# Kernel tuning notes

Hardware: AMD Instinct MI355X
Metric: run time of the kernel (lower is better)

## Reference

```python
import jax, jax.numpy as jnp
import numpy as np

E = 16          # num_experts
H = 2048        # hidden_size
I = 768         # moe_intermediate_size
T = 2048        # tokens (batch*seq)
K = 2           # top_k


def setup_inputs() -> dict:
    key = jax.random.key(0)
    k1, k2, k3, k4, k5 = jax.random.split(key, 5)
    hidden_states = jax.random.normal(k1, (T, H), dtype=jnp.float32)
    top_k_index = jax.random.randint(k2, (T, K), 0, E, dtype=jnp.int32)
    w = jax.random.uniform(k3, (T, K), dtype=jnp.float32)
    top_k_weights = w / jnp.sum(w, axis=-1, keepdims=True)  # softmax-like router weights
    init_std = 0.02
    gate_up_proj = jax.random.normal(k4, (E, 2 * I, H), dtype=jnp.float32) * init_std
    down_proj = jax.random.normal(k5, (E, H, I), dtype=jnp.float32) * init_std
    return {
        "hidden_states": hidden_states,
        "top_k_index": top_k_index,
        "top_k_weights": top_k_weights,
        "gate_up_proj": gate_up_proj,
        "down_proj": down_proj,
    }


def reference(hidden_states, top_k_index, top_k_weights, gate_up_proj, down_proj):
    # Combine matrix C[t, e] = sum_k top_k_weights[t, k] * 1[top_k_index[t,k] == e]
    # Tokens not routed to expert e get weight 0, so the dense-masked compute
    # below is mathematically identical to the per-expert gather/scatter loop.
    t_idx = jnp.arange(T)[:, None]
    C = jnp.zeros((T, E), dtype=hidden_states.dtype).at[t_idx, top_k_index].add(top_k_weights)

    # gate/up projection for every (token, expert): [T, E, 2I]
    gu = jnp.einsum('th,egh->teg', hidden_states, gate_up_proj)
    gate, up = jnp.split(gu, 2, axis=-1)                  # [T, E, I] each
    mid = jax.nn.silu(gate) * up                          # SwiGLU, [T, E, I]
    # down projection fused with routed combine weights -> [T, H]
    out = jnp.einsum('tei,ehi,te->th', mid, down_proj, C)
    return out
```

## Files before the change

### kernel.cpp

```cpp
#include <hip/hip_runtime.h>

#define TTOK  2048
#define HID   2048
#define IMID  768
#define NEXP  16
#define NPAIR 4096
#define NSLOT 4224
#define BM    128
#define BK    64
#define MAXT  48
#define ABUF  (128 * 64)

#define GUP_CHUNKS 24576
#define DN_CHUNKS  12288

typedef __attribute__((ext_vector_type(8))) short  short8;
typedef __attribute__((ext_vector_type(4))) float  floatx4;

__device__ __forceinline__ unsigned pk2(float a, float b) {
    union { float f; unsigned u; } x{a}, y{b};
    unsigned ra = (x.u + 0x7FFFu + ((x.u >> 16) & 1u)) >> 16;
    unsigned rb = (y.u + 0x7FFFu + ((y.u >> 16) & 1u)) & 0xFFFF0000u;
    return ra | rb;
}

__device__ __forceinline__ short f2bf(float f) {
    union { float f; unsigned u; } v; v.f = f;
    return (short)((v.u + 0x7FFFu + ((v.u >> 16) & 1u)) >> 16);
}

__device__ __forceinline__ short8 cvt8(float4 a, float4 b) {
    union { unsigned u[4]; short8 s; } r;
    r.u[0] = pk2(a.x, a.y); r.u[1] = pk2(a.z, a.w);
    r.u[2] = pk2(b.x, b.y); r.u[3] = pk2(b.z, b.w);
    return r.s;
}

__device__ __forceinline__ void async_cp16(const void* g, void* l) {
    __builtin_amdgcn_global_load_lds(
        (const __attribute__((address_space(1))) void*)g,
        (__attribute__((address_space(3))) void*)l, 16, 0, 0);
}

__global__ __launch_bounds__(256) void k_pre(
    const float* __restrict__ hs, const int* __restrict__ idx,
    const float* __restrict__ tkw, const float* __restrict__ gup,
    const float* __restrict__ down, int* __restrict__ ntiles,
    int4* __restrict__ tiles, int* __restrict__ tok,
    float* __restrict__ wgt, short* __restrict__ X,
    short* __restrict__ gupb, short* __restrict__ downb)
{
    const int tid = threadIdx.x;
    const int bx  = (int)blockIdx.x;
    if (bx == 0) {
        __shared__ int cnt[NEXP], cur[NEXP];
        if (tid < NEXP) cnt[tid] = 0;
        __syncthreads();
        for (int i = tid; i < NPAIR; i += 256) atomicAdd(&cnt[idx[i]], 1);
        __syncthreads();
        if (tid == 0) {
            int s = 0, nt = 0;
            for (int e = 0; e < NEXP; e++) {
                cur[e] = s;
                int n = cnt[e];
                for (int tt = 0; tt * BM < n; tt++) {
                    tiles[nt] = make_int4(e, s + tt * BM, min(BM, n - tt * BM), 0);
                    nt++;
                }
                s += n;
            }
            *ntiles = nt;
        }
        __syncthreads();
        for (int i = tid; i < NPAIR; i += 256) {
            int e = idx[i];
            int p = atomicAdd(&cur[e], 1);
            tok[p] = i >> 1;
            wgt[p] = tkw[i];
        }
        for (int i = NPAIR + tid; i < NSLOT; i += 256) { tok[i] = 0; wgt[i] = 0.0f; }
    } else if (bx <= TTOK) {
        const int row = bx - 1;
        const float* src = hs + (size_t)row * HID + tid * 8;
        float4 a = *(const float4*)src;
        float4 b = *(const float4*)(src + 4);
        *(short8*)(X + (size_t)row * HID + tid * 8) = cvt8(a, b);
    } else if (bx <= TTOK + GUP_CHUNKS) {
        const size_t c = (size_t)(bx - 1 - TTOK);
        const float* src = gup + c * 2048 + tid * 8;
        float4 a = *(const float4*)src;
        float4 b = *(const float4*)(src + 4);
        *(short8*)(gupb + c * 2048 + tid * 8) = cvt8(a, b);
    } else {
        const size_t c = (size_t)(bx - 1 - TTOK - GUP_CHUNKS);
        const float* src = down + c * 2048 + tid * 8;
        float4 a = *(const float4*)src;
        float4 b = *(const float4*)(src + 4);
        *(short8*)(downb + c * 2048 + tid * 8) = cvt8(a, b);
    }
}

__global__ __launch_bounds__(256, 2) void k_gemm1(
    const short* __restrict__ gupb, const short* __restrict__ X,
    const int* __restrict__ ntiles, const int4* __restrict__ tiles,
    const int* __restrict__ tok, const float* __restrict__ wgt,
    short* __restrict__ mid)
{
    if ((int)blockIdx.y >= *ntiles) return;
    const int4 td = tiles[blockIdx.y];
    const int e = td.x, rowstart = td.y, nvalid = td.z;
    const int ct = blockIdx.x;

    __shared__ short sA[2 * ABUF];
    __shared__ short sB[2 * ABUF];
    __shared__ int   s_tok[BM];
    __shared__ float s_w[BM];

    const int tid = threadIdx.x;
    if (tid < BM) { s_tok[tid] = tok[rowstart + tid]; s_w[tid] = wgt[rowstart + tid]; }
    __syncthreads();

    const int wave = tid >> 6, lane = tid & 63;
    const int m16 = lane & 15, quad = lane >> 4;

    const int lrow = tid >> 3;
    const int gsw  = (tid & 7) ^ (lrow & 7);
    const short* aga[4];
    const short* bga[4];
#pragma unroll
    for (int j = 0; j < 4; j++)
        aga[j] = X + (size_t)s_tok[lrow + j * 32] * HID + gsw * 8;
    const short* gb = gupb + (size_t)e * (2 * IMID) * HID + gsw * 8;
#pragma unroll
    for (int j = 0; j < 2; j++) {
        bga[j]     = gb + (size_t)(ct * 64 + lrow + j * 32) * HID;
        bga[j + 2] = gb + (size_t)(IMID + ct * 64 + lrow + j * 32) * HID;
    }

    auto stage = [&](int k0, short* dA, short* dB) {
#pragma unroll
        for (int j = 0; j < 4; j++)
            async_cp16(aga[j] + k0, dA + j * 2048 + wave * 512);
#pragma unroll
        for (int j = 0; j < 4; j++)
            async_cp16(bga[j] + k0, dB + j * 2048 + wave * 512);
    };

    const int Wm = (wave >> 1) << 6;
    const int Wi = (wave & 1) << 5;
    floatx4 ag[4][2], au[4][2];
#pragma unroll
    for (int a = 0; a < 4; a++)
#pragma unroll
        for (int b = 0; b < 2; b++) { ag[a][b] = (floatx4)0.0f; au[a][b] = (floatx4)0.0f; }

    stage(0, sA, sB);
    __syncthreads();

    const int nsteps = HID / BK;
    for (int ks = 0; ks < nsteps; ks++) {
        const short* Acur = sA + (ks & 1) * ABUF;
        const short* Bcur = sB + (ks & 1) * ABUF;
        if (ks + 1 < nsteps)
            stage((ks + 1) * BK, sA + ((ks + 1) & 1) * ABUF, sB + ((ks + 1) & 1) * ABUF);

#pragma unroll
        for (int h = 0; h < 2; h++) {
            short8 af[4];
#pragma unroll
            for (int mf = 0; mf < 4; mf++) {
                int row = Wm + mf * 16 + m16;
                int gc = (h * 4 + quad) ^ (row & 7);
                af[mf] = *(const short8*)&Acur[row * 64 + gc * 8];
            }
#pragma unroll
            for (int nf = 0; nf < 2; nf++) {
                int brow = Wi + nf * 16 + m16;
                int gcb = (h * 4 + quad) ^ (brow & 7);
                const short8 bg = *(const short8*)&Bcur[brow * 64 + gcb * 8];
                const short8 bu = *(const short8*)&Bcur[(64 + brow) * 64 + gcb * 8];
#pragma unroll
                for (int mf = 0; mf < 4; mf++) {
                    ag[mf][nf] = __builtin_amdgcn_mfma_f32_16x16x32_bf16(af[mf], bg, ag[mf][nf], 0, 0, 0);
                    au[mf][nf] = __builtin_amdgcn_mfma_f32_16x16x32_bf16(af[mf], bu, au[mf][nf], 0, 0, 0);
                }
            }
        }
        __syncthreads();
    }

#pragma unroll
    for (int mf = 0; mf < 4; mf++) {
#pragma unroll
        for (int r = 0; r < 4; r++) {
            int m = Wm + mf * 16 + quad * 4 + r;
            if (m < nvalid) {
                float w = s_w[m];
                size_t rowp = (size_t)(rowstart + m) * IMID + ct * 64;
#pragma unroll
                for (int nf = 0; nf < 2; nf++) {
                    float g = ag[mf][nf][r], u = au[mf][nf][r];
                    float val = g / (1.0f + __expf(-g)) * u * w;
                    mid[rowp + Wi + nf * 16 + m16] = f2bf(val);
                }
            }
        }
    }
}

__global__ __launch_bounds__(256, 2) void k_gemm2(
    const short* __restrict__ downb, const short* __restrict__ mid,
    const int* __restrict__ ntiles, const int4* __restrict__ tiles,
    const int* __restrict__ tok, float* __restrict__ out)
{
    if ((int)blockIdx.y >= *ntiles) return;
    const int4 td = tiles[blockIdx.y];
    const int e = td.x, rowstart = td.y, nvalid = td.z;
    const int ct = blockIdx.x;

    __shared__ short sA[2 * ABUF];
    __shared__ short sB[2 * ABUF];
    __shared__ int   s_tok[BM];

    const int tid = threadIdx.x;
    if (tid < BM) s_tok[tid] = tok[rowstart + tid];
    __syncthreads();

    const int wave = tid >> 6, lane = tid & 63;
    const int m16 = lane & 15, quad = lane >> 4;

    const int lrow = tid >> 3;
    const int gsw  = (tid & 7) ^ (lrow & 7);
    const short* aga[4];
    const short* bga[4];
#pragma unroll
    for (int j = 0; j < 4; j++)
        aga[j] = mid + (size_t)(rowstart + lrow + j * 32) * IMID + gsw * 8;
    const short* db = downb + ((size_t)e * HID + ct * 128) * IMID + gsw * 8;
#pragma unroll
    for (int j = 0; j < 4; j++)
        bga[j] = db + (size_t)(lrow + j * 32) * IMID;

    auto stage = [&](int k0, short* dA, short* dB) {
#pragma unroll
        for (int j = 0; j < 4; j++)
            async_cp16(aga[j] + k0, dA + j * 2048 + wave * 512);
#pragma unroll
        for (int j = 0; j < 4; j++)
            async_cp16(bga[j] + k0, dB + j * 2048 + wave * 512);
    };

    const int Wm = (wave >> 1) << 6;
    const int Wn = (wave & 1) << 6;
    floatx4 acc[4][4];
#pragma unroll
    for (int a = 0; a < 4; a++)
#pragma unroll
        for (int b = 0; b < 4; b++) acc[a][b] = (floatx4)0.0f;

    stage(0, sA, sB);
    __syncthreads();

    const int nsteps = IMID / BK;
    for (int ks = 0; ks < nsteps; ks++) {
        const short* Acur = sA + (ks & 1) * ABUF;
        const short* Bcur = sB + (ks & 1) * ABUF;
        if (ks + 1 < nsteps)
            stage((ks + 1) * BK, sA + ((ks + 1) & 1) * ABUF, sB + ((ks + 1) & 1) * ABUF);

#pragma unroll
        for (int h = 0; h < 2; h++) {
            short8 af[4];
#pragma unroll
            for (int mf = 0; mf < 4; mf++) {
                int row = Wm + mf * 16 + m16;
                int gc = (h * 4 + quad) ^ (row & 7);
                af[mf] = *(const short8*)&Acur[row * 64 + gc * 8];
            }
#pragma unroll
            for (int nf = 0; nf < 4; nf++) {
                int brow = Wn + nf * 16 + m16;
                int gcb = (h * 4 + quad) ^ (brow & 7);
                const short8 bf_ = *(const short8*)&Bcur[brow * 64 + gcb * 8];
#pragma unroll
                for (int mf = 0; mf < 4; mf++)
                    acc[mf][nf] = __builtin_amdgcn_mfma_f32_16x16x32_bf16(af[mf], bf_, acc[mf][nf], 0, 0, 0);
            }
        }
        __syncthreads();
    }

#pragma unroll
    for (int mf = 0; mf < 4; mf++) {
#pragma unroll
        for (int r = 0; r < 4; r++) {
            int m = Wm + mf * 16 + quad * 4 + r;
            if (m < nvalid) {
                int t = s_tok[m];
                float* op = out + (size_t)t * HID + ct * 128;
#pragma unroll
                for (int nf = 0; nf < 4; nf++)
                    atomicAdd(op + Wn + nf * 16 + m16, acc[mf][nf][r]);
            }
        }
    }
}

extern "C" void kernel_launch(void* const* d_in, const int* in_sizes, int n_in,
                              void* d_out, int out_size, void* d_ws, size_t ws_size,
                              hipStream_t stream) {
    const float* hs   = (const float*)d_in[0];
    const int*   idx  = (const int*)d_in[1];
    const float* tkw  = (const float*)d_in[2];
    const float* gup  = (const float*)d_in[3];
    const float* down = (const float*)d_in[4];
    float* out = (float*)d_out;

    char* ws = (char*)d_ws;
    int*   ntiles = (int*)ws;
    int4*  tiles  = (int4*)(ws + 16);
    int*   tok    = (int*)(ws + 1024);
    float* wgt    = (float*)(ws + 1024 + NSLOT * 4);
    short* mid    = (short*)(ws + 36864);
    short* X      = (short*)(ws + 36864 + (size_t)NSLOT * IMID * 2);
    short* gupb   = (short*)(ws + (16u << 20));
    short* downb  = (short*)(ws + (16u << 20) + (size_t)NEXP * 2 * IMID * HID * 2);

    hipMemsetAsync(d_out, 0, (size_t)TTOK * HID * sizeof(float), stream);
    k_pre  <<<1 + TTOK + GUP_CHUNKS + DN_CHUNKS, 256, 0, stream>>>(
        hs, idx, tkw, gup, down, ntiles, tiles, tok, wgt, X, gupb, downb);
    k_gemm1<<<dim3(IMID / 64, MAXT), 256, 0, stream>>>(gupb, X, ntiles, tiles, tok, wgt, mid);
    k_gemm2<<<dim3(HID / 128, MAXT), 256, 0, stream>>>(downb, mid, ntiles, tiles, tok, out);
}
```

Measured before the change: 484.0 us.

## Use grid-stride conversion kernel and explicit vmcnt waits with raw barriers in GEMMs

The fp32-to-bf16 preprocessing kernel changes from one block per 2048-element chunk (about 39k blocks) to a fixed 2048-block grid-stride loop over all three tensors. Both grouped GEMM loops replace __syncthreads with explicit s_waitcnt vmcnt(8)/vmcnt(0) plus s_barrier and sched_barrier. This lets the prefetch of the next K tile stay in flight while waiting only for the current tile's async LDS loads. The aim is to cut block-launch overhead and over-conservative waits, but correctness now depends on the hand-set vmcnt count matching the 8 async copies per stage.

```diff
diff --git a/kernel.cpp b/kernel.cpp
--- a/kernel.cpp
+++ b/kernel.cpp
@@ -11,8 +11,10 @@
 #define MAXT  48
 #define ABUF  (128 * 64)
 
-#define GUP_CHUNKS 24576
-#define DN_CHUNKS  12288
+#define HS_U   524288u
+#define GUP_U  6291456u
+#define DN_U   3145728u
+#define NU_TOT (HS_U + GUP_U + DN_U)
 
 typedef __attribute__((ext_vector_type(8))) short  short8;
 typedef __attribute__((ext_vector_type(4))) float  floatx4;
@@ -51,8 +53,7 @@
     short* __restrict__ gupb, short* __restrict__ downb)
 {
     const int tid = threadIdx.x;
-    const int bx  = (int)blockIdx.x;
-    if (bx == 0) {
+    if (blockIdx.x == 0) {
         __shared__ int cnt[NEXP], cur[NEXP];
         if (tid < NEXP) cnt[tid] = 0;
         __syncthreads();
@@ -79,24 +80,18 @@
             wgt[p] = tkw[i];
         }
         for (int i = NPAIR + tid; i < NSLOT; i += 256) { tok[i] = 0; wgt[i] = 0.0f; }
-    } else if (bx <= TTOK) {
-        const int row = bx - 1;
-        const float* src = hs + (size_t)row * HID + tid * 8;
-        float4 a = *(const float4*)src;
-        float4 b = *(const float4*)(src + 4);
-        *(short8*)(X + (size_t)row * HID + tid * 8) = cvt8(a, b);
-    } else if (bx <= TTOK + GUP_CHUNKS) {
-        const size_t c = (size_t)(bx - 1 - TTOK);
-        const float* src = gup + c * 2048 + tid * 8;
-        float4 a = *(const float4*)src;
-        float4 b = *(const float4*)(src + 4);
-        *(short8*)(gupb + c * 2048 + tid * 8) = cvt8(a, b);
-    } else {
-        const size_t c = (size_t)(bx - 1 - TTOK - GUP_CHUNKS);
-        const float* src = down + c * 2048 + tid * 8;
-        float4 a = *(const float4*)src;
-        float4 b = *(const float4*)(src + 4);
-        *(short8*)(downb + c * 2048 + tid * 8) = cvt8(a, b);
+        return;
+    }
+    const unsigned nthr = (gridDim.x - 1) * 256u;
+    unsigned u = (blockIdx.x - 1) * 256u + tid;
+    for (; u < NU_TOT; u += nthr) {
+        const float* src; short* dst; unsigned off;
+        if (u < HS_U)              { src = hs;   dst = X;     off = u; }
+        else if (u < HS_U + GUP_U) { src = gup;  dst = gupb;  off = u - HS_U; }
+        else                       { src = down; dst = downb; off = u - HS_U - GUP_U; }
+        float4 a = *((const float4*)src + (size_t)2 * off);
+        float4 b = *((const float4*)src + (size_t)2 * off + 1);
+        *((short8*)dst + off) = cvt8(a, b);
     }
 }
 
@@ -155,14 +150,19 @@
         for (int b = 0; b < 2; b++) { ag[a][b] = (floatx4)0.0f; au[a][b] = (floatx4)0.0f; }
 
     stage(0, sA, sB);
-    __syncthreads();
 
     const int nsteps = HID / BK;
     for (int ks = 0; ks < nsteps; ks++) {
         const short* Acur = sA + (ks & 1) * ABUF;
         const short* Bcur = sB + (ks & 1) * ABUF;
-        if (ks + 1 < nsteps)
+        if (ks + 1 < nsteps) {
             stage((ks + 1) * BK, sA + ((ks + 1) & 1) * ABUF, sB + ((ks + 1) & 1) * ABUF);
+            asm volatile("s_waitcnt vmcnt(8)" ::: "memory");
+        } else {
+            asm volatile("s_waitcnt vmcnt(0)" ::: "memory");
+        }
+        __builtin_amdgcn_s_barrier();
+        __builtin_amdgcn_sched_barrier(0);
 
 #pragma unroll
         for (int h = 0; h < 2; h++) {
@@ -186,7 +186,8 @@
                 }
             }
         }
-        __syncthreads();
+        __builtin_amdgcn_sched_barrier(0);
+        __builtin_amdgcn_s_barrier();
     }
 
 #pragma unroll
@@ -259,14 +260,19 @@
         for (int b = 0; b < 4; b++) acc[a][b] = (floatx4)0.0f;
 
     stage(0, sA, sB);
-    __syncthreads();
 
     const int nsteps = IMID / BK;
     for (int ks = 0; ks < nsteps; ks++) {
         const short* Acur = sA + (ks & 1) * ABUF;
         const short* Bcur = sB + (ks & 1) * ABUF;
-        if (ks + 1 < nsteps)
+        if (ks + 1 < nsteps) {
             stage((ks + 1) * BK, sA + ((ks + 1) & 1) * ABUF, sB + ((ks + 1) & 1) * ABUF);
+            asm volatile("s_waitcnt vmcnt(8)" ::: "memory");
+        } else {
+            asm volatile("s_waitcnt vmcnt(0)" ::: "memory");
+        }
+        __builtin_amdgcn_s_barrier();
+        __builtin_amdgcn_sched_barrier(0);
 
 #pragma unroll
         for (int h = 0; h < 2; h++) {
@@ -287,7 +293,8 @@
                     acc[mf][nf] = __builtin_amdgcn_mfma_f32_16x16x32_bf16(af[mf], bf_, acc[mf][nf], 0, 0, 0);
             }
         }
-        __syncthreads();
+        __builtin_amdgcn_sched_barrier(0);
+        __builtin_amdgcn_s_barrier();
     }
 
 #pragma unroll
@@ -327,7 +334,7 @@
     short* downb  = (short*)(ws + (16u << 20) + (size_t)NEXP * 2 * IMID * HID * 2);
 
     hipMemsetAsync(d_out, 0, (size_t)TTOK * HID * sizeof(float), stream);
-    k_pre  <<<1 + TTOK + GUP_CHUNKS + DN_CHUNKS, 256, 0, stream>>>(
+    k_pre  <<<2049, 256, 0, stream>>>(
         hs, idx, tkw, gup, down, ntiles, tiles, tok, wgt, X, gupb, downb);
     k_gemm1<<<dim3(IMID / 64, MAXT), 256, 0, stream>>>(gupb, X, ntiles, tiles, tok, wgt, mid);
     k_gemm2<<<dim3(HID / 128, MAXT), 256, 0, stream>>>(downb, mid, ntiles, tiles, tok, out);
```

After: 476.5 us. About the same (-1.5%).
